# Performance work log

Measured on AMD Instinct MI355X. Metric: run time of the kernel, lower is better.

The kernel has to match this reference:

```python
import jax, jax.numpy as jnp
import numpy as np

W_CHAMFER = (1.0, 1.0, 1.0)
W_LAPLACE = 0.5
W_MOVE = 0.1
W_EDGE = 0.1
W_NORMAL = 1.6e-4
W_CONST = 1.0
LAP_CONST = (0.2, 1.0, 1.0)
EPS = 1e-12


def _normalize(x):
    # F.normalize(x, dim=-1): x / max(||x||, eps)
    n = jnp.sqrt(jnp.sum(x * x, axis=-1, keepdims=True))
    return x / jnp.maximum(n, EPS)


def _pairwise_sq(x, y):
    # x: (B,N,3), y: (B,M,3) -> (B,N,M) squared distances, GEMM form
    x2 = jnp.sum(x * x, -1)
    y2 = jnp.sum(y * y, -1)
    xy = jnp.einsum('bnd,bmd->bnm', x, y)
    return x2[:, :, None] + y2[:, None, :] - 2.0 * xy


def _laplace_coord(pts, lap_idx):
    # pts: (B,V,3); lap_idx: (V,10) = [8 neighbor idx (-1 invalid), self, count]
    idx = lap_idx[:, :8]
    mask = idx < 0
    safe = jnp.where(mask, 0, idx)
    nbrs = pts[:, safe]                                  # (B,V,8,3)
    nbrs = jnp.where(mask[None, :, :, None], 0.0, nbrs)
    count = lap_idx[:, -1].astype(pts.dtype)
    return pts - nbrs.sum(2) / count[None, :, None]


def setup_inputs():
    key = jax.random.key(0)
    B, M = 2, 8192
    Vs = (642, 2562, 10242)
    Es = (1920, 7680, 30720)
    ks = jax.random.split(key, 3 + 4 * 3)
    inp = {}
    inp['gt_coord'] = jax.random.normal(ks[0], (B, M, 3), jnp.float32)
    inp['gt_normal'] = _normalize(jax.random.normal(ks[1], (B, M, 3), jnp.float32))
    for i, (V, E) in enumerate(zip(Vs, Es)):
        k0, k1, k2, k3 = ks[3 + 4 * i], ks[4 + 4 * i], ks[5 + 4 * i], ks[6 + 4 * i]
        inp[f'pred_coord_{i}'] = jax.random.normal(k0, (B, V, 3), jnp.float32)
        inp[f'pred_before_{i}'] = inp[f'pred_coord_{i}'] + 0.05 * jax.random.normal(k1, (B, V, 3), jnp.float32)
        inp[f'edges_{i}'] = jax.random.randint(k2, (E, 2), 0, V)
        nbr = jax.random.randint(k3, (V, 8), 0, V)
        nbr = nbr.at[:, 6:].set(-1)                      # 6 valid neighbors, 2 invalid slots
        self_idx = jnp.arange(V)[:, None]
        count = jnp.full((V, 1), 6)
        inp[f'laplace_idx_{i}'] = jnp.concatenate([nbr, self_idx, count], axis=1)
    return inp


def reference(pred_coord_0, pred_coord_1, pred_coord_2, pred_before_0, pred_before_1, pred_before_2, gt_coord, gt_normal, laplace_idx_0, laplace_idx_1, laplace_idx_2, edges_0, edges_1, edges_2):
    preds = (pred_coord_0, pred_coord_1, pred_coord_2)
    befores = (pred_before_0, pred_before_1, pred_before_2)
    laps = (laplace_idx_0, laplace_idx_1, laplace_idx_2)
    edges_all = (edges_0, edges_1, edges_2)
    chamfer_loss = 0.0
    edge_loss = 0.0
    normal_loss = 0.0
    lap_loss = 0.0
    move_loss = 0.0
    for i in range(3):
        pred, before, lap_idx, edges = preds[i], befores[i], laps[i], edges_all[i]
        # shared pairwise distance matrix for chamfer + knn (original recomputes)
        d = _pairwise_sq(pred, gt_coord)                 # (B,V,M)
        chamfer_loss = chamfer_loss + W_CHAMFER[i] * (jnp.mean(jnp.min(d, axis=1)) + jnp.mean(jnp.min(d, axis=2)))
        knn_idx = jnp.argmin(d, axis=2)                  # (B,V): nearest gt per pred pt
        e0, e1 = edges[:, 0], edges[:, 1]
        evec = _normalize(pred[:, e0] - pred[:, e1])     # (B,E,3)
        # faithful to torch: knn.idx.flatten() then index_select -> only batch-0
        # indices ever selected since edge ids < V
        sel = knn_idx.reshape(-1)[e0]
        nrm = _normalize(gt_normal[:, sel])              # (B,E,3)
        normal_loss = normal_loss + jnp.mean(jnp.abs(jnp.sum(evec * nrm, axis=2)))
        edge_loss = edge_loss + 3.0 * jnp.mean((pred[:, e0] - pred[:, e1]) ** 2)
        l1 = _laplace_coord(before, lap_idx)
        l2 = _laplace_coord(pred, lap_idx)
        lap_loss = lap_loss + LAP_CONST[i] * 3.0 * jnp.mean((l1 - l2) ** 2)
        if i > 0:
            move_loss = move_loss + LAP_CONST[i] * 3.0 * jnp.mean((before - pred) ** 2)
    loss = chamfer_loss + W_LAPLACE * lap_loss + W_MOVE * move_loss + W_EDGE * edge_loss + W_NORMAL * normal_loss
    return W_CONST * loss
```

## Files before the change

kernel.cpp:

```cpp
#include <hip/hip_runtime.h>


#define DEV __device__ __forceinline__

DEV unsigned int ford(float f) {
    unsigned int u = __float_as_uint(f);
    return (u & 0x80000000u) ? ~u : (u | 0x80000000u);
}
DEV float funord(unsigned int o) {
    unsigned int u = (o & 0x80000000u) ? (o ^ 0x80000000u) : ~o;
    return __uint_as_float(u);
}
DEV unsigned long long umin64(unsigned long long a, unsigned long long b) { return a < b ? a : b; }

DEV float blockReduceSum256(float v) {
    #pragma unroll
    for (int o = 32; o > 0; o >>= 1) v += __shfl_down(v, o, 64);
    __shared__ float red4[4];
    int wid = threadIdx.x >> 6;
    if ((threadIdx.x & 63) == 0) red4[wid] = v;
    __syncthreads();
    return (threadIdx.x == 0) ? (red4[0] + red4[1] + red4[2] + red4[3]) : 0.0f;
}

template<bool STORE, bool ARGMIN>
DEV void roleA(int a, const float* p0, const float* p1, const float* p2,
               const float* gt, char* ws, char* smem)
{
    const int b = ARGMIN ? 0 : 1;
    int vtG = a >> 5, mc = a & 31;
    int lvl, vtL, V; const float* predL;
    if (vtG == 0)      { lvl = 0; vtL = 0;       V = 642;   predL = p0; }
    else if (vtG < 4)  { lvl = 1; vtL = vtG - 1; V = 2562;  predL = p1; }
    else               { lvl = 2; vtL = vtG - 4; V = 10242; predL = p2; }
    int tid = threadIdx.x, lane = tid & 63, w = tid >> 6;
    float4* SG = (float4*)smem;
    int mbase = mc << 8;
    {
        int m = mbase + tid;
        const float* gp = gt + ((size_t)b * 8192 + m) * 3;
        float gx = gp[0], gy = gp[1], gz = gp[2];
        SG[tid] = make_float4(-2.f * gx, -2.f * gy, -2.f * gz, fmaf(gx, gx, fmaf(gy, gy, gz * gz)));
    }
    float px[14], py[14], pz[14];
    #pragma unroll
    for (int r = 0; r < 14; r++) {
        int vr = vtL * 896 + r * 64 + lane;
        int v = vr - (vr >= V ? V : 0);
        const float* pp = predL + ((size_t)b * V + v) * 3;
        px[r] = pp[0]; py[r] = pp[1]; pz[r] = pp[2];
    }
    __syncthreads();
    if (ARGMIN) {
        float best[14]; int bi[14];
        #pragma unroll
        for (int r = 0; r < 14; r++) { best[r] = 3.0e38f; bi[r] = 0; }
        #pragma unroll 4
        for (int i = 0; i < 64; i++) {
            int j = (w << 6) + i;
            float4 q = SG[j];
            int cand = mbase + j;
            #pragma unroll
            for (int r = 0; r < 14; r++) {
                float d = fmaf(q.x, px[r], fmaf(q.y, py[r], fmaf(q.z, pz[r], q.w)));
                if (d < best[r]) { best[r] = d; bi[r] = cand; }
            }
        }
        unsigned long long* RED = (unsigned long long*)(smem + 4096);
        #pragma unroll
        for (int r = 0; r < 14; r++)
            RED[w * 896 + r * 64 + lane] = ((unsigned long long)ford(best[r]) << 32) | (unsigned)bi[r];
        __syncthreads();
        for (int s = tid; s < 896; s += 256) {
            unsigned long long mm = umin64(umin64(RED[s], RED[s + 896]),
                                           umin64(RED[s + 1792], RED[s + 2688]));
            if (STORE) {
                ((unsigned long long*)(ws + 54808))[((size_t)(vtG * 896 + s)) * 32 + mc] = mm;
            } else {
                int vr = vtL * 896 + s; int v = vr - (vr >= V ? V : 0);
                int lvlOff = (lvl == 0) ? 0 : (lvl == 1 ? 642 : 3204);
                atomicMin((unsigned long long*)(ws + 54808) + (lvlOff + v), mm);
            }
        }
    } else {
        float best[14];
        #pragma unroll
        for (int r = 0; r < 14; r++) best[r] = 3.0e38f;
        #pragma unroll 2
        for (int i = 0; i < 64; i += 2) {
            int j = (w << 6) + i;
            float4 q0 = SG[j], q1 = SG[j + 1];
            #pragma unroll
            for (int r = 0; r < 14; r++) {
                float d0 = fmaf(q0.x, px[r], fmaf(q0.y, py[r], fmaf(q0.z, pz[r], q0.w)));
                float d1 = fmaf(q1.x, px[r], fmaf(q1.y, py[r], fmaf(q1.z, pz[r], q1.w)));
                best[r] = fminf(fminf(best[r], d0), d1);
            }
        }
        unsigned* RED = (unsigned*)(smem + 4096);
        #pragma unroll
        for (int r = 0; r < 14; r++)
            RED[w * 896 + r * 64 + lane] = ford(best[r]);
        __syncthreads();
        for (int s = tid; s < 896; s += 256) {
            unsigned mm = min(min(RED[s], RED[s + 896]), min(RED[s + 1792], RED[s + 2688]));
            if (STORE) {
                ((unsigned*)(ws + 3724824))[((size_t)(vtG * 896 + s)) * 32 + mc] = mm;
            } else {
                int vr = vtL * 896 + s; int v = vr - (vr >= V ? V : 0);
                int lvlOff = (lvl == 0) ? 0 : (lvl == 1 ? 642 : 3204);
                atomicMin((unsigned*)(ws + 162376) + (lvlOff + v), mm);
            }
        }
    }
}

template<bool STORE>
DEV void roleB(int i, const float* p0, const float* p1, const float* p2,
               const float* gt, char* ws, char* smem)
{
    int lvl, V, cc, t, lvlB, baseB;
    if (i < 32)       { lvl = 0; V = 642;   cc = 2;  t = i;       lvlB = 0;     baseB = 0; }
    else if (i < 128) { lvl = 1; V = 2562;  cc = 6;  t = i - 32;  lvlB = 16384; baseB = 32768; }
    else              { lvl = 2; V = 10242; cc = 21; t = i - 128; lvlB = 32768; baseB = 131072; }
    const float* predL = lvl == 0 ? p0 : (lvl == 1 ? p1 : p2);
    int c = t % cc; int rest = t / cc; int mt = rest & 7; int b = rest >> 3;
    int tid = threadIdx.x, lane = tid & 63, w = tid >> 6;
    float4* SP = (float4*)smem;
    int vbase = c * 512;
    #pragma unroll
    for (int k = 0; k < 2; k++) {
        int j = tid + k * 256, v = vbase + j;
        if (v < V) {
            const float* pp = predL + ((size_t)b * V + v) * 3;
            float x = pp[0], y = pp[1], z = pp[2];
            SP[j] = make_float4(-2.f * x, -2.f * y, -2.f * z, fmaf(x, x, fmaf(y, y, z * z)));
        } else SP[j] = make_float4(0.f, 0.f, 0.f, 3.0e38f);
    }
    float gx[16], gy[16], gz[16];
    #pragma unroll
    for (int r = 0; r < 16; r++) {
        int m = mt * 1024 + r * 64 + lane;
        const float* gp = gt + ((size_t)b * 8192 + m) * 3;
        gx[r] = gp[0]; gy[r] = gp[1]; gz[r] = gp[2];
    }
    __syncthreads();
    float best[16];
    #pragma unroll
    for (int r = 0; r < 16; r++) best[r] = 3.0e38f;
    #pragma unroll 2
    for (int i2 = 0; i2 < 128; i2 += 2) {
        int j = (w << 7) + i2;
        float4 q0 = SP[j], q1 = SP[j + 1];
        #pragma unroll
        for (int r = 0; r < 16; r++) {
            float d0 = fmaf(q0.x, gx[r], fmaf(q0.y, gy[r], fmaf(q0.z, gz[r], q0.w)));
            float d1 = fmaf(q1.x, gx[r], fmaf(q1.y, gy[r], fmaf(q1.z, gz[r], q1.w)));
            best[r] = fminf(fminf(best[r], d0), d1);
        }
    }
    unsigned* RED = (unsigned*)(smem + 8192);
    #pragma unroll
    for (int r = 0; r < 16; r++)
        RED[w * 1024 + r * 64 + lane] = ford(best[r]);
    __syncthreads();
    for (int s = tid; s < 1024; s += 256) {
        unsigned mm = min(min(RED[s], RED[s + 1024]), min(RED[s + 2048], RED[s + 3072]));
        int m = mt * 1024 + s;
        if (STORE) ((unsigned*)(ws + 5559832))[baseB + (size_t)((b << 13) + m) * cc + c] = mm;
        else       atomicMin((unsigned*)(ws + 216160) + (lvlB + (b << 13) + m), mm);
    }
}

template<bool STORE>
__global__ __launch_bounds__(256, 3) void kMega(
    const float* __restrict__ p0, const float* __restrict__ p1, const float* __restrict__ p2,
    const float* __restrict__ b0p, const float* __restrict__ b1p, const float* __restrict__ b2p,
    const int* __restrict__ l0, const int* __restrict__ l1, const int* __restrict__ l2,
    const float* __restrict__ gt, char* ws)
{
    extern __shared__ char smem[];
    int bid = blockIdx.x;
    if (bid == 0 && threadIdx.x == 0) { *(float*)ws = 0.f; *(unsigned*)(ws + 4) = 0u; }
    if (bid < 128) {
        float c = 0.0f;
        int idx = bid * 256 + threadIdx.x;
        if (idx < 26892) {
            int level, V, t;
            const float *pred, *bef; const int* lap;
            if (idx < 1284)      { level = 0; V = 642;   pred = p0; bef = b0p; lap = l0; t = idx; }
            else if (idx < 6408) { level = 1; V = 2562;  pred = p1; bef = b1p; lap = l1; t = idx - 1284; }
            else                 { level = 2; V = 10242; pred = p2; bef = b2p; lap = l2; t = idx - 6408; }
            int b = t / V;
            int v = t - b * V;
            const float* P  = pred + ((size_t)b * V + v) * 3;
            const float* Bf = bef  + ((size_t)b * V + v) * 3;
            float dx = Bf[0] - P[0], dy = Bf[1] - P[1], dz = Bf[2] - P[2];
            float sx = 0.f, sy = 0.f, sz = 0.f;
            const int* L = lap + v * 10;
            #pragma unroll
            for (int j = 0; j < 8; j++) {
                int n = L[j];
                if (n >= 0) {
                    const float* Pn = pred + ((size_t)b * V + n) * 3;
                    const float* Bn = bef  + ((size_t)b * V + n) * 3;
                    sx += Bn[0] - Pn[0]; sy += Bn[1] - Pn[1]; sz += Bn[2] - Pn[2];
                }
            }
            float invc = 1.0f / (float)L[9];
            float lx = dx - sx * invc, ly = dy - sy * invc, lz = dz - sz * invc;
            float sl = fmaf(lx, lx, fmaf(ly, ly, lz * lz));
            float sm = fmaf(dx, dx, fmaf(dy, dy, dz * dz));
            float lapc = (level == 0) ? 0.2f : 1.0f;
            float iBV = 1.0f / (2.0f * (float)V);
            c = sl * (0.5f * lapc * iBV) + ((level > 0) ? sm * (0.1f * lapc * iBV) : 0.0f);
        }
        c = blockReduceSum256(c);
        if (threadIdx.x == 0) ((float*)(ws + 8))[bid] = c;
    }
    else if (bid < 592)  roleB<STORE>(bid - 128, p0, p1, p2, gt, ws, smem);
    else if (bid < 1104) roleA<STORE, true >(bid - 592,  p0, p1, p2, gt, ws, smem);
    else                 roleA<STORE, false>(bid - 1104, p0, p1, p2, gt, ws, smem);
}

template<bool STORE>
__global__ __launch_bounds__(256) void kCombine(
    const float* __restrict__ p0, const float* __restrict__ p1, const float* __restrict__ p2,
    const float* __restrict__ gt, char* ws)
{
    int bid = blockIdx.x, tid = threadIdx.x;
    float c = 0.0f;
    if (bid == 304) {
        if (tid < 128) c = ((float*)(ws + 8))[tid];
    } else {
        int idx = bid * 256 + tid;
        if (idx < 28672) {
            int b = idx / 14336;
            int q = idx % 14336;
            int vtG = q / 896, s = q % 896;
            int lvl, vtL, V; const float* predL; int lvlOff; float inv;
            if (vtG == 0)     { lvl = 0; vtL = 0;       V = 642;   predL = p0; lvlOff = 0;    inv = 1.f / 1284.f; }
            else if (vtG < 4) { lvl = 1; vtL = vtG - 1; V = 2562;  predL = p1; lvlOff = 642;  inv = 1.f / 5124.f; }
            else              { lvl = 2; vtL = vtG - 4; V = 10242; predL = p2; lvlOff = 3204; inv = 1.f / 20484.f; }
            int vr = vtL * 896 + s;
            if (vr < V) {
                float d; unsigned idxm = 0;
                if (STORE) {
                    if (b == 0) {
                        const unsigned long long* P = (const unsigned long long*)(ws + 54808)
                                                      + ((size_t)(vtG * 896 + s)) * 32;
                        unsigned long long mm = ~0ull;
                        #pragma unroll 8
                        for (int k = 0; k < 32; k++) mm = umin64(mm, P[k]);
                        d = funord((unsigned)(mm >> 32)); idxm = (unsigned)mm;
                    } else {
                        const unsigned* P = (const unsigned*)(ws + 3724824)
                                            + ((size_t)(vtG * 896 + s)) * 32;
                        unsigned mm = 0xFFFFFFFFu;
                        #pragma unroll 8
                        for (int k = 0; k < 32; k++) mm = min(mm, P[k]);
                        d = funord(mm);
                    }
                } else {
                    if (b == 0) {
                        unsigned long long mm = ((unsigned long long*)(ws + 54808))[lvlOff + vr];
                        d = funord((unsigned)(mm >> 32)); idxm = (unsigned)mm;
                    } else {
                        d = funord(((unsigned*)(ws + 162376))[lvlOff + vr]);
                    }
                }
                const float* pp = predL + ((size_t)b * V + vr) * 3;
                c = (d + fmaf(pp[0], pp[0], fmaf(pp[1], pp[1], pp[2] * pp[2]))) * inv;
                if (b == 0) ((int*)(ws + 1024))[lvlOff + vr] = (int)idxm;
            }
        } else if (idx < 77824) {
            int jj = idx - 28672;
            int lvl = jj >> 14, r = jj & 16383;
            int cc = lvl == 0 ? 2 : (lvl == 1 ? 6 : 21);
            int baseB = lvl == 0 ? 0 : (lvl == 1 ? 32768 : 131072);
            float d;
            if (STORE) {
                const unsigned* P = (const unsigned*)(ws + 5559832) + baseB + (size_t)r * cc;
                unsigned mm = 0xFFFFFFFFu;
                for (int k = 0; k < cc; k++) mm = min(mm, P[k]);
                d = funord(mm);
            } else {
                d = funord(((const unsigned*)(ws + 216160))[(lvl << 14) + r]);
            }
            const float* gp = gt + (size_t)r * 3;
            c = (d + fmaf(gp[0], gp[0], fmaf(gp[1], gp[1], gp[2] * gp[2]))) * (1.f / 16384.f);
        }
    }
    c = blockReduceSum256(c);
    if (tid == 0) atomicAdd((float*)ws, c);
}

__global__ __launch_bounds__(256) void kEdgeOut(
    const float* __restrict__ p0, const float* __restrict__ p1, const float* __restrict__ p2,
    const int* __restrict__ e0p, const int* __restrict__ e1p, const int* __restrict__ e2p,
    const float* __restrict__ gtn, char* ws, float* __restrict__ out)
{
    const int* knn = (const int*)(ws + 1024);
    int idx = blockIdx.x * 256 + threadIdx.x;
    float c = 0.0f;
    {
        int E, V, lvlOff, t;
        const float* pred; const int* edges;
        if (idx < 3840)       { E = 1920;  V = 642;   lvlOff = 0;    pred = p0; edges = e0p; t = idx; }
        else if (idx < 19200) { E = 7680;  V = 2562;  lvlOff = 642;  pred = p1; edges = e1p; t = idx - 3840; }
        else                  { E = 30720; V = 10242; lvlOff = 3204; pred = p2; edges = e2p; t = idx - 19200; }
        int b = t / E;
        int e = t % E;
        int a0 = edges[e * 2 + 0];
        int a1 = edges[e * 2 + 1];
        const float* P = pred + (size_t)b * V * 3;
        float dx = P[a0 * 3 + 0] - P[a1 * 3 + 0];
        float dy = P[a0 * 3 + 1] - P[a1 * 3 + 1];
        float dz = P[a0 * 3 + 2] - P[a1 * 3 + 2];
        float sq = fmaf(dx, dx, fmaf(dy, dy, dz * dz));
        float inv = 1.0f / fmaxf(sqrtf(sq), 1e-12f);
        int sel = knn[lvlOff + a0];
        const float* nr = gtn + ((size_t)b * 8192 + sel) * 3;
        float nx = nr[0], ny = nr[1], nz = nr[2];
        float invn = 1.0f / fmaxf(sqrtf(fmaf(nx, nx, fmaf(ny, ny, nz * nz))), 1e-12f);
        float dotv = fmaf(dx, nx, fmaf(dy, ny, dz * nz)) * inv * invn;
        float iBE = 1.0f / (2.0f * (float)E);
        c = sq * (0.1f * iBE) + fabsf(dotv) * (0.00016f * iBE);
    }
    c = blockReduceSum256(c);
    if (threadIdx.x == 0) {
        atomicAdd((float*)ws, c);
        __threadfence();
        unsigned t = atomicAdd((unsigned*)(ws + 4), 1u);
        if (t == 314u) out[0] = atomicAdd((float*)ws, 0.0f);
    }
}

extern "C" void kernel_launch(void* const* d_in, const int* in_sizes, int n_in,
                              void* d_out, int out_size, void* d_ws, size_t ws_size,
                              hipStream_t stream) {
    const float *gt, *gtn, *pred[3], *bef[3];
    const int *edg[3], *lapx[3];
    if (in_sizes[0] == 49152) {
        gt  = (const float*)d_in[0];
        gtn = (const float*)d_in[1];
        for (int i = 0; i < 3; i++) {
            pred[i] = (const float*)d_in[2 + 4 * i];
            bef[i]  = (const float*)d_in[3 + 4 * i];
            edg[i]  = (const int*)  d_in[4 + 4 * i];
            lapx[i] = (const int*)  d_in[5 + 4 * i];
        }
    } else {
        for (int i = 0; i < 3; i++) pred[i] = (const float*)d_in[i];
        for (int i = 0; i < 3; i++) bef[i]  = (const float*)d_in[3 + i];
        gt  = (const float*)d_in[6];
        gtn = (const float*)d_in[7];
        for (int i = 0; i < 3; i++) lapx[i] = (const int*)d_in[8 + i];
        for (int i = 0; i < 3; i++) edg[i]  = (const int*)d_in[11 + i];
    }

    char* ws = (char*)d_ws;
    bool store = ws_size >= (size_t)7460376;

    if (store) {
        kMega<true><<<1616, 256, 32768, stream>>>(pred[0], pred[1], pred[2],
                                                  bef[0], bef[1], bef[2],
                                                  lapx[0], lapx[1], lapx[2], gt, ws);
        kCombine<true><<<305, 256, 0, stream>>>(pred[0], pred[1], pred[2], gt, ws);
    } else {
        hipMemsetAsync(ws + 54808, 0xFF, 412768 - 54808, stream);
        kMega<false><<<1616, 256, 32768, stream>>>(pred[0], pred[1], pred[2],
                                                   bef[0], bef[1], bef[2],
                                                   lapx[0], lapx[1], lapx[2], gt, ws);
        kCombine<false><<<305, 256, 0, stream>>>(pred[0], pred[1], pred[2], gt, ws);
    }
    kEdgeOut<<<315, 256, 0, stream>>>(pred[0], pred[1], pred[2],
                                      edg[0], edg[1], edg[2], gtn, ws, (float*)d_out);
}
```

Baseline: 138.4 us.

## Compute chamfer distances with bf16x3-split MFMA and embedded argmin codes

The FP32 FMA pairwise-distance loops for both chamfer directions are replaced by bf16 MFMA instructions. Each coordinate is split into three bf16 parts so the dot-product keeps near-FP32 precision, and the squared norms are folded into the K dimension. The argmin index for batch 0 is coarsely embedded in the low mantissa bits of the min value and then refined in the combine kernel by rechecking 4 candidates in exact FP32. The workspace layout and tiling are reorganised around this. The change risks small precision differences and relies on the float bit-embedding trick to stay correct.

```diff
diff --git a/kernel.cpp b/kernel.cpp
--- a/kernel.cpp
+++ b/kernel.cpp
@@ -3,15 +3,8 @@
 
 #define DEV __device__ __forceinline__
 
-DEV unsigned int ford(float f) {
-    unsigned int u = __float_as_uint(f);
-    return (u & 0x80000000u) ? ~u : (u | 0x80000000u);
-}
-DEV float funord(unsigned int o) {
-    unsigned int u = (o & 0x80000000u) ? (o ^ 0x80000000u) : ~o;
-    return __uint_as_float(u);
-}
-DEV unsigned long long umin64(unsigned long long a, unsigned long long b) { return a < b ? a : b; }
+typedef __attribute__((ext_vector_type(8))) short bs8;
+typedef __attribute__((ext_vector_type(4))) float f32x4;
 
 DEV float blockReduceSum256(float v) {
     #pragma unroll
@@ -23,157 +16,93 @@
     return (threadIdx.x == 0) ? (red4[0] + red4[1] + red4[2] + red4[3]) : 0.0f;
 }
 
-template<bool STORE, bool ARGMIN>
-DEV void roleA(int a, const float* p0, const float* p1, const float* p2,
-               const float* gt, char* ws, char* smem)
+DEV void split3(float u, unsigned short& h, unsigned short& m, unsigned short& l) {
+    unsigned a = __float_as_uint(u);
+    h = (unsigned short)(a >> 16);
+    float r1 = u - __uint_as_float(a & 0xFFFF0000u);
+    unsigned bb = __float_as_uint(r1);
+    m = (unsigned short)(bb >> 16);
+    float r2 = r1 - __uint_as_float(bb & 0xFFFF0000u);
+    l = (unsigned short)(__float_as_uint(r2) >> 16);
+}
+
+DEV void packGT(const float* __restrict__ gp, char* dst) {
+    float x = gp[0], y = gp[1], z = gp[2];
+    unsigned short hx,mx,lx, hy,my,ly, hz,mz,lz, nh,nm,nl;
+    split3(x,hx,mx,lx); split3(y,hy,my,ly); split3(z,hz,mz,lz);
+    float n = fmaf(x,x,fmaf(y,y,z*z));
+    split3(n,nh,nm,nl);
+    const short ONE = (short)0x3F80;
+    bs8 w0 = {(short)hx,(short)hx,(short)mx,(short)hx,(short)lx,(short)mx,(short)hy,(short)hy};
+    bs8 w1 = {(short)my,(short)hy,(short)ly,(short)my,(short)hz,(short)hz,(short)mz,(short)hz};
+    bs8 w2 = {(short)lz,(short)mz,(short)nh,(short)nm,(short)nl,ONE,ONE,ONE};
+    bs8 w3 = {0,0,0,0,0,0,0,0};
+    *(bs8*)(dst)       = w0;
+    *(bs8*)(dst + 256) = w1;
+    *(bs8*)(dst + 512) = w2;
+    *(bs8*)(dst + 768) = w3;
+}
+
+DEV void packVERT(const float* __restrict__ pp, char* dst) {
+    float x = pp[0], y = pp[1], z = pp[2];
+    unsigned short hx,mx,lx, hy,my,ly, hz,mz,lz, nh,nm,nl;
+    split3(-2.f*x,hx,mx,lx); split3(-2.f*y,hy,my,ly); split3(-2.f*z,hz,mz,lz);
+    float n = fmaf(x,x,fmaf(y,y,z*z));
+    split3(n,nh,nm,nl);
+    const short ONE = (short)0x3F80;
+    bs8 w0 = {(short)hx,(short)mx,(short)hx,(short)lx,(short)hx,(short)mx,(short)hy,(short)my};
+    bs8 w1 = {(short)hy,(short)ly,(short)hy,(short)my,(short)hz,(short)mz,(short)hz,(short)lz};
+    bs8 w2 = {(short)hz,(short)mz,ONE,ONE,ONE,(short)nh,(short)nm,(short)nl};
+    bs8 w3 = {0,0,0,0,0,0,0,0};
+    *(bs8*)(dst)       = w0;
+    *(bs8*)(dst + 256) = w1;
+    *(bs8*)(dst + 512) = w2;
+    *(bs8*)(dst + 768) = w3;
+}
+
+template<bool B0>
+DEV void mfmaLoop(const char* SA, const char* SB, char* VML,
+                  float (&gmin)[8][4], int embedBase, unsigned embedMask)
 {
-    const int b = ARGMIN ? 0 : 1;
-    int vtG = a >> 5, mc = a & 31;
-    int lvl, vtL, V; const float* predL;
-    if (vtG == 0)      { lvl = 0; vtL = 0;       V = 642;   predL = p0; }
-    else if (vtG < 4)  { lvl = 1; vtL = vtG - 1; V = 2562;  predL = p1; }
-    else               { lvl = 2; vtL = vtG - 4; V = 10242; predL = p2; }
-    int tid = threadIdx.x, lane = tid & 63, w = tid >> 6;
-    float4* SG = (float4*)smem;
-    int mbase = mc << 8;
-    {
-        int m = mbase + tid;
-        const float* gp = gt + ((size_t)b * 8192 + m) * 3;
-        float gx = gp[0], gy = gp[1], gz = gp[2];
-        SG[tid] = make_float4(-2.f * gx, -2.f * gy, -2.f * gz, fmaf(gx, gx, fmaf(gy, gy, gz * gz)));
-    }
-    float px[14], py[14], pz[14];
-    #pragma unroll
-    for (int r = 0; r < 14; r++) {
-        int vr = vtL * 896 + r * 64 + lane;
-        int v = vr - (vr >= V ? V : 0);
-        const float* pp = predL + ((size_t)b * V + v) * 3;
-        px[r] = pp[0]; py[r] = pp[1]; pz[r] = pp[2];
-    }
-    __syncthreads();
-    if (ARGMIN) {
-        float best[14]; int bi[14];
+    const int tid = threadIdx.x;
+    const int w = tid >> 6, L = tid & 63, lr = L & 15, lg = L >> 4;
+    const char* abase = SA + (w * 8) * 1024 + lg * 256 + lr * 16;
+    bs8 af[8];
+    #pragma unroll
+    for (int g = 0; g < 8; g++) af[g] = *(const bs8*)(abase + g * 1024);
+    const f32x4 zero = {0.f, 0.f, 0.f, 0.f};
+    const char* bbase = SB + lg * 256 + lr * 16;
+    bs8 bf = *(const bs8*)(bbase);
+    #pragma unroll 2
+    for (int vg = 0; vg < 16; vg++) {
+        bs8 bfn = bf;
+        if (vg < 15) bfn = *(const bs8*)(bbase + (vg + 1) * 1024);
+        float vmin = 3.0e38f;
+        int code = embedBase;
         #pragma unroll
-        for (int r = 0; r < 14; r++) { best[r] = 3.0e38f; bi[r] = 0; }
-        #pragma unroll 4
-        for (int i = 0; i < 64; i++) {
-            int j = (w << 6) + i;
-            float4 q = SG[j];
-            int cand = mbase + j;
-            #pragma unroll
-            for (int r = 0; r < 14; r++) {
-                float d = fmaf(q.x, px[r], fmaf(q.y, py[r], fmaf(q.z, pz[r], q.w)));
-                if (d < best[r]) { best[r] = d; bi[r] = cand; }
-            }
-        }
-        unsigned long long* RED = (unsigned long long*)(smem + 4096);
-        #pragma unroll
-        for (int r = 0; r < 14; r++)
-            RED[w * 896 + r * 64 + lane] = ((unsigned long long)ford(best[r]) << 32) | (unsigned)bi[r];
-        __syncthreads();
-        for (int s = tid; s < 896; s += 256) {
-            unsigned long long mm = umin64(umin64(RED[s], RED[s + 896]),
-                                           umin64(RED[s + 1792], RED[s + 2688]));
-            if (STORE) {
-                ((unsigned long long*)(ws + 54808))[((size_t)(vtG * 896 + s)) * 32 + mc] = mm;
-            } else {
-                int vr = vtL * 896 + s; int v = vr - (vr >= V ? V : 0);
-                int lvlOff = (lvl == 0) ? 0 : (lvl == 1 ? 642 : 3204);
-                atomicMin((unsigned long long*)(ws + 54808) + (lvlOff + v), mm);
-            }
-        }
-    } else {
-        float best[14];
-        #pragma unroll
-        for (int r = 0; r < 14; r++) best[r] = 3.0e38f;
-        #pragma unroll 2
-        for (int i = 0; i < 64; i += 2) {
-            int j = (w << 6) + i;
-            float4 q0 = SG[j], q1 = SG[j + 1];
-            #pragma unroll
-            for (int r = 0; r < 14; r++) {
-                float d0 = fmaf(q0.x, px[r], fmaf(q0.y, py[r], fmaf(q0.z, pz[r], q0.w)));
-                float d1 = fmaf(q1.x, px[r], fmaf(q1.y, py[r], fmaf(q1.z, pz[r], q1.w)));
-                best[r] = fminf(fminf(best[r], d0), d1);
-            }
-        }
-        unsigned* RED = (unsigned*)(smem + 4096);
-        #pragma unroll
-        for (int r = 0; r < 14; r++)
-            RED[w * 896 + r * 64 + lane] = ford(best[r]);
-        __syncthreads();
-        for (int s = tid; s < 896; s += 256) {
-            unsigned mm = min(min(RED[s], RED[s + 896]), min(RED[s + 1792], RED[s + 2688]));
-            if (STORE) {
-                ((unsigned*)(ws + 3724824))[((size_t)(vtG * 896 + s)) * 32 + mc] = mm;
-            } else {
-                int vr = vtL * 896 + s; int v = vr - (vr >= V ? V : 0);
-                int lvlOff = (lvl == 0) ? 0 : (lvl == 1 ? 642 : 3204);
-                atomicMin((unsigned*)(ws + 162376) + (lvlOff + v), mm);
-            }
-        }
+        for (int gg = 0; gg < 8; gg++) {
+            f32x4 acc = __builtin_amdgcn_mfma_f32_16x16x32_bf16(af[gg], bf, zero, 0, 0, 0);
+            gmin[gg][0] = fminf(gmin[gg][0], acc[0]);
+            gmin[gg][1] = fminf(gmin[gg][1], acc[1]);
+            gmin[gg][2] = fminf(gmin[gg][2], acc[2]);
+            gmin[gg][3] = fminf(gmin[gg][3], acc[3]);
+            float t = fminf(fminf(fminf(acc[0], acc[1]), acc[2]), acc[3]);
+            if (B0) {
+                t = fmaxf(t, 0.0f);
+                t = __uint_as_float((__float_as_uint(t) & embedMask) | (unsigned)code);
+                code += 4;
+            }
+            vmin = fminf(vmin, t);
+        }
+        vmin = fminf(vmin, __shfl_xor(vmin, 16));
+        vmin = fminf(vmin, __shfl_xor(vmin, 32));
+        if (lg == 0) *(float*)(VML + ((vg * 16 + lr) * 4 + w) * 4) = vmin;
+        bf = bfn;
     }
 }
 
 template<bool STORE>
-DEV void roleB(int i, const float* p0, const float* p1, const float* p2,
-               const float* gt, char* ws, char* smem)
-{
-    int lvl, V, cc, t, lvlB, baseB;
-    if (i < 32)       { lvl = 0; V = 642;   cc = 2;  t = i;       lvlB = 0;     baseB = 0; }
-    else if (i < 128) { lvl = 1; V = 2562;  cc = 6;  t = i - 32;  lvlB = 16384; baseB = 32768; }
-    else              { lvl = 2; V = 10242; cc = 21; t = i - 128; lvlB = 32768; baseB = 131072; }
-    const float* predL = lvl == 0 ? p0 : (lvl == 1 ? p1 : p2);
-    int c = t % cc; int rest = t / cc; int mt = rest & 7; int b = rest >> 3;
-    int tid = threadIdx.x, lane = tid & 63, w = tid >> 6;
-    float4* SP = (float4*)smem;
-    int vbase = c * 512;
-    #pragma unroll
-    for (int k = 0; k < 2; k++) {
-        int j = tid + k * 256, v = vbase + j;
-        if (v < V) {
-            const float* pp = predL + ((size_t)b * V + v) * 3;
-            float x = pp[0], y = pp[1], z = pp[2];
-            SP[j] = make_float4(-2.f * x, -2.f * y, -2.f * z, fmaf(x, x, fmaf(y, y, z * z)));
-        } else SP[j] = make_float4(0.f, 0.f, 0.f, 3.0e38f);
-    }
-    float gx[16], gy[16], gz[16];
-    #pragma unroll
-    for (int r = 0; r < 16; r++) {
-        int m = mt * 1024 + r * 64 + lane;
-        const float* gp = gt + ((size_t)b * 8192 + m) * 3;
-        gx[r] = gp[0]; gy[r] = gp[1]; gz[r] = gp[2];
-    }
-    __syncthreads();
-    float best[16];
-    #pragma unroll
-    for (int r = 0; r < 16; r++) best[r] = 3.0e38f;
-    #pragma unroll 2
-    for (int i2 = 0; i2 < 128; i2 += 2) {
-        int j = (w << 7) + i2;
-        float4 q0 = SP[j], q1 = SP[j + 1];
-        #pragma unroll
-        for (int r = 0; r < 16; r++) {
-            float d0 = fmaf(q0.x, gx[r], fmaf(q0.y, gy[r], fmaf(q0.z, gz[r], q0.w)));
-            float d1 = fmaf(q1.x, gx[r], fmaf(q1.y, gy[r], fmaf(q1.z, gz[r], q1.w)));
-            best[r] = fminf(fminf(best[r], d0), d1);
-        }
-    }
-    unsigned* RED = (unsigned*)(smem + 8192);
-    #pragma unroll
-    for (int r = 0; r < 16; r++)
-        RED[w * 1024 + r * 64 + lane] = ford(best[r]);
-    __syncthreads();
-    for (int s = tid; s < 1024; s += 256) {
-        unsigned mm = min(min(RED[s], RED[s + 1024]), min(RED[s + 2048], RED[s + 3072]));
-        int m = mt * 1024 + s;
-        if (STORE) ((unsigned*)(ws + 5559832))[baseB + (size_t)((b << 13) + m) * cc + c] = mm;
-        else       atomicMin((unsigned*)(ws + 216160) + (lvlB + (b << 13) + m), mm);
-    }
-}
-
-template<bool STORE>
-__global__ __launch_bounds__(256, 3) void kMega(
+__global__ __launch_bounds__(256, 3) void kMega2(
     const float* __restrict__ p0, const float* __restrict__ p1, const float* __restrict__ p2,
     const float* __restrict__ b0p, const float* __restrict__ b1p, const float* __restrict__ b2p,
     const int* __restrict__ l0, const int* __restrict__ l1, const int* __restrict__ l2,
@@ -197,17 +126,17 @@
             const float* Bf = bef  + ((size_t)b * V + v) * 3;
             float dx = Bf[0] - P[0], dy = Bf[1] - P[1], dz = Bf[2] - P[2];
             float sx = 0.f, sy = 0.f, sz = 0.f;
-            const int* L = lap + v * 10;
+            const int* Lp = lap + v * 10;
             #pragma unroll
             for (int j = 0; j < 8; j++) {
-                int n = L[j];
+                int n = Lp[j];
                 if (n >= 0) {
                     const float* Pn = pred + ((size_t)b * V + n) * 3;
                     const float* Bn = bef  + ((size_t)b * V + n) * 3;
                     sx += Bn[0] - Pn[0]; sy += Bn[1] - Pn[1]; sz += Bn[2] - Pn[2];
                 }
             }
-            float invc = 1.0f / (float)L[9];
+            float invc = 1.0f / (float)Lp[9];
             float lx = dx - sx * invc, ly = dy - sy * invc, lz = dz - sz * invc;
             float sl = fmaf(lx, lx, fmaf(ly, ly, lz * lz));
             float sm = fmaf(dx, dx, fmaf(dy, dy, dz * dz));
@@ -217,78 +146,157 @@
         }
         c = blockReduceSum256(c);
         if (threadIdx.x == 0) ((float*)(ws + 8))[bid] = c;
-    }
-    else if (bid < 592)  roleB<STORE>(bid - 128, p0, p1, p2, gt, ws, smem);
-    else if (bid < 1104) roleA<STORE, true >(bid - 592,  p0, p1, p2, gt, ws, smem);
-    else                 roleA<STORE, false>(bid - 1104, p0, p1, p2, gt, ws, smem);
+        return;
+    }
+    int cid = bid - 128;
+    int gtt = cid & 15;
+    int t2 = cid >> 4;
+    int b = t2 >= 55 ? 1 : 0;
+    int vt = t2 - 55 * b;
+    int lvl, V, vtl; const float* predL;
+    if (vt < 3)       { lvl = 0; V = 642;   vtl = vt;      predL = p0; }
+    else if (vt < 14) { lvl = 1; V = 2562;  vtl = vt - 3;  predL = p1; }
+    else              { lvl = 2; V = 10242; vtl = vt - 14; predL = p2; }
+    char* SA  = smem;
+    char* SB  = smem + 32768;
+    char* VML = smem + 49152;
+    int tid = threadIdx.x;
+    {
+        int v = vtl * 256 + tid;
+        if (v >= V) v -= V;
+        packVERT(predL + ((size_t)b * V + v) * 3, SB + (tid >> 4) * 1024 + (tid & 15) * 16);
+    }
+    #pragma unroll
+    for (int k = 0; k < 2; k++) {
+        int j = tid + k * 256;
+        packGT(gt + ((size_t)b * 8192 + gtt * 512 + j) * 3, SA + (j >> 4) * 1024 + (j & 15) * 16);
+    }
+    __syncthreads();
+    float gmin[8][4];
+    #pragma unroll
+    for (int g = 0; g < 8; g++) {
+        gmin[g][0] = 3.0e38f; gmin[g][1] = 3.0e38f; gmin[g][2] = 3.0e38f; gmin[g][3] = 3.0e38f;
+    }
+    int w = tid >> 6, L = tid & 63, lg = L >> 4;
+    if (b == 0) {
+        unsigned mask = STORE ? 0xFFFFFF80u : 0xFFFFF800u;
+        int eb = w * 32 + lg + (STORE ? 0 : (gtt << 7));
+        mfmaLoop<true>(SA, SB, VML, gmin, eb, mask);
+    } else {
+        mfmaLoop<false>(SA, SB, VML, gmin, 0, 0u);
+    }
+    __syncthreads();
+    float* GML = (float*)SA;
+    #pragma unroll
+    for (int gg = 0; gg < 8; gg++) {
+        #pragma unroll
+        for (int r = 0; r < 4; r++)
+            GML[(w * 128 + gg * 16 + lg * 4 + r) * 16 + (L & 15)] = gmin[gg][r];
+    }
+    __syncthreads();
+    {
+        float4 vv = *(float4*)(VML + tid * 16);
+        float pv = fminf(fminf(vv.x, vv.y), fminf(vv.z, vv.w));
+        int padOff = lvl == 0 ? 0 : (lvl == 1 ? 768 : 3584);
+        int vs = b * 14080 + padOff + vtl * 256 + tid;
+        if (STORE) {
+            ((float*)(ws + 54808))[(size_t)gtt * 28160 + vs] = pv;
+        } else {
+            int v = vtl * 256 + tid;
+            if (v < V) atomicMin((unsigned*)(ws + 54808) + vs, __float_as_uint(fmaxf(pv, 0.0f)));
+        }
+    }
+    {
+        int tb = lvl == 0 ? 0 : (lvl == 1 ? 3 : 14);
+        #pragma unroll
+        for (int k = 0; k < 2; k++) {
+            int g = tid + k * 256;
+            float q = 3.0e38f;
+            #pragma unroll
+            for (int cc = 0; cc < 16; cc++)
+                q = fminf(q, GML[g * 16 + ((cc + tid) & 15)]);
+            if (STORE) {
+                ((float*)(ws + 1857048))[(size_t)(b * 55 + tb + vtl) * 8192 + gtt * 512 + g] = q;
+            } else {
+                atomicMin((unsigned*)(ws + 167448) + (((b * 3 + lvl) << 13) + gtt * 512 + g),
+                          __float_as_uint(fmaxf(q, 0.0f)));
+            }
+        }
+    }
 }
 
 template<bool STORE>
-__global__ __launch_bounds__(256) void kCombine(
+__global__ __launch_bounds__(256) void kCombine2(
     const float* __restrict__ p0, const float* __restrict__ p1, const float* __restrict__ p2,
     const float* __restrict__ gt, char* ws)
 {
     int bid = blockIdx.x, tid = threadIdx.x;
     float c = 0.0f;
-    if (bid == 304) {
+    if (bid == 302) {
         if (tid < 128) c = ((float*)(ws + 8))[tid];
     } else {
         int idx = bid * 256 + tid;
-        if (idx < 28672) {
-            int b = idx / 14336;
-            int q = idx % 14336;
-            int vtG = q / 896, s = q % 896;
-            int lvl, vtL, V; const float* predL; int lvlOff; float inv;
-            if (vtG == 0)     { lvl = 0; vtL = 0;       V = 642;   predL = p0; lvlOff = 0;    inv = 1.f / 1284.f; }
-            else if (vtG < 4) { lvl = 1; vtL = vtG - 1; V = 2562;  predL = p1; lvlOff = 642;  inv = 1.f / 5124.f; }
-            else              { lvl = 2; vtL = vtG - 4; V = 10242; predL = p2; lvlOff = 3204; inv = 1.f / 20484.f; }
-            int vr = vtL * 896 + s;
-            if (vr < V) {
-                float d; unsigned idxm = 0;
+        if (idx < 28160) {
+            int b = idx >= 14080 ? 1 : 0;
+            int q = idx - b * 14080;
+            int lvl, V, lvlOff, padOff; const float* predL; float inv;
+            if (q < 768)       { lvl=0; V=642;   padOff=0;    lvlOff=0;    predL=p0; inv=1.f/1284.f; }
+            else if (q < 3584) { lvl=1; V=2562;  padOff=768;  lvlOff=642;  predL=p1; inv=1.f/5124.f; }
+            else               { lvl=2; V=10242; padOff=3584; lvlOff=3204; predL=p2; inv=1.f/20484.f; }
+            int v = q - padOff;
+            if (v < V) {
+                float best; int bt = 0; unsigned bits;
                 if (STORE) {
-                    if (b == 0) {
-                        const unsigned long long* P = (const unsigned long long*)(ws + 54808)
-                                                      + ((size_t)(vtG * 896 + s)) * 32;
-                        unsigned long long mm = ~0ull;
-                        #pragma unroll 8
-                        for (int k = 0; k < 32; k++) mm = umin64(mm, P[k]);
-                        d = funord((unsigned)(mm >> 32)); idxm = (unsigned)mm;
-                    } else {
-                        const unsigned* P = (const unsigned*)(ws + 3724824)
-                                            + ((size_t)(vtG * 896 + s)) * 32;
-                        unsigned mm = 0xFFFFFFFFu;
-                        #pragma unroll 8
-                        for (int k = 0; k < 32; k++) mm = min(mm, P[k]);
-                        d = funord(mm);
+                    const float* P = (const float*)(ws + 54808) + idx;
+                    best = P[0];
+                    #pragma unroll
+                    for (int t = 1; t < 16; t++) {
+                        float u = P[(size_t)t * 28160];
+                        if (u < best) { best = u; bt = t; }
                     }
+                    bits = __float_as_uint(best);
                 } else {
-                    if (b == 0) {
-                        unsigned long long mm = ((unsigned long long*)(ws + 54808))[lvlOff + vr];
-                        d = funord((unsigned)(mm >> 32)); idxm = (unsigned)mm;
-                    } else {
-                        d = funord(((unsigned*)(ws + 162376))[lvlOff + vr]);
+                    bits = ((const unsigned*)(ws + 54808))[idx];
+                    best = __uint_as_float(bits);
+                    bt = (bits >> 7) & 15;
+                }
+                float d;
+                if (b == 0) {
+                    int code = bits & 0x7F;
+                    int m0 = bt * 512 + code * 4;
+                    const float* pp = predL + (size_t)v * 3;
+                    float px = pp[0], py = pp[1], pz = pp[2];
+                    float bd = 3.0e38f; int bm = m0;
+                    #pragma unroll
+                    for (int u2 = 0; u2 < 4; u2++) {
+                        const float* gp = gt + (size_t)(m0 + u2) * 3;
+                        float dx = px - gp[0], dy = py - gp[1], dz = pz - gp[2];
+                        float dd = fmaf(dx, dx, fmaf(dy, dy, dz * dz));
+                        if (dd < bd) { bd = dd; bm = m0 + u2; }
                     }
+                    ((int*)(ws + 1024))[lvlOff + v] = bm;
+                    d = bd;
+                } else {
+                    d = best;
                 }
-                const float* pp = predL + ((size_t)b * V + vr) * 3;
-                c = (d + fmaf(pp[0], pp[0], fmaf(pp[1], pp[1], pp[2] * pp[2]))) * inv;
-                if (b == 0) ((int*)(ws + 1024))[lvlOff + vr] = (int)idxm;
-            }
-        } else if (idx < 77824) {
-            int jj = idx - 28672;
-            int lvl = jj >> 14, r = jj & 16383;
-            int cc = lvl == 0 ? 2 : (lvl == 1 ? 6 : 21);
-            int baseB = lvl == 0 ? 0 : (lvl == 1 ? 32768 : 131072);
+                c = d * inv;
+            }
+        } else if (idx < 77312) {
+            int r = idx - 28160;
+            int b = r >= 24576 ? 1 : 0;
+            int rem = r - b * 24576;
+            int lvl = rem >> 13, m = rem & 8191;
             float d;
             if (STORE) {
-                const unsigned* P = (const unsigned*)(ws + 5559832) + baseB + (size_t)r * cc;
-                unsigned mm = 0xFFFFFFFFu;
-                for (int k = 0; k < cc; k++) mm = min(mm, P[k]);
-                d = funord(mm);
+                int nt = lvl == 0 ? 3 : (lvl == 1 ? 11 : 41);
+                int tb = lvl == 0 ? 0 : (lvl == 1 ? 3 : 14);
+                const float* P = (const float*)(ws + 1857048) + (size_t)(b * 55 + tb) * 8192 + m;
+                d = P[0];
+                for (int k2 = 1; k2 < nt; k2++) d = fminf(d, P[(size_t)k2 * 8192]);
             } else {
-                d = funord(((const unsigned*)(ws + 216160))[(lvl << 14) + r]);
-            }
-            const float* gp = gt + (size_t)r * 3;
-            c = (d + fmaf(gp[0], gp[0], fmaf(gp[1], gp[1], gp[2] * gp[2]))) * (1.f / 16384.f);
+                d = __uint_as_float(((const unsigned*)(ws + 167448))[((b * 3 + lvl) << 13) + m]);
+            }
+            c = d * (1.f / 16384.f);
         }
     }
     c = blockReduceSum256(c);
@@ -360,19 +368,19 @@
     }
 
     char* ws = (char*)d_ws;
-    bool store = ws_size >= (size_t)7460376;
+    bool store = ws_size >= (size_t)5461528;
 
     if (store) {
-        kMega<true><<<1616, 256, 32768, stream>>>(pred[0], pred[1], pred[2],
-                                                  bef[0], bef[1], bef[2],
-                                                  lapx[0], lapx[1], lapx[2], gt, ws);
-        kCombine<true><<<305, 256, 0, stream>>>(pred[0], pred[1], pred[2], gt, ws);
-    } else {
-        hipMemsetAsync(ws + 54808, 0xFF, 412768 - 54808, stream);
-        kMega<false><<<1616, 256, 32768, stream>>>(pred[0], pred[1], pred[2],
+        kMega2<true><<<1888, 256, 53248, stream>>>(pred[0], pred[1], pred[2],
                                                    bef[0], bef[1], bef[2],
                                                    lapx[0], lapx[1], lapx[2], gt, ws);
-        kCombine<false><<<305, 256, 0, stream>>>(pred[0], pred[1], pred[2], gt, ws);
+        kCombine2<true><<<303, 256, 0, stream>>>(pred[0], pred[1], pred[2], gt, ws);
+    } else {
+        hipMemsetAsync(ws + 54808, 0xFF, 364056 - 54808, stream);
+        kMega2<false><<<1888, 256, 53248, stream>>>(pred[0], pred[1], pred[2],
+                                                    bef[0], bef[1], bef[2],
+                                                    lapx[0], lapx[1], lapx[2], gt, ws);
+        kCombine2<false><<<303, 256, 0, stream>>>(pred[0], pred[1], pred[2], gt, ws);
     }
     kEdgeOut<<<315, 256, 0, stream>>>(pred[0], pred[1], pred[2],
                                       edg[0], edg[1], edg[2], gtn, ws, (float*)d_out);
```

Measured after the change: 131.0 us. -5.4%, faster.
